# Performance work log

Measured on AMD Instinct MI355X. Metric: run time of the kernel, lower is better.

## Reference

```python
import jax, jax.numpy as jnp
import numpy as np
from jax import lax


def setup_inputs() -> dict:
    key = jax.random.key(0)
    ks = jax.random.split(key, 6)
    B, C, H, W, K = 4, 4, 64, 64, 8192
    return {
        "x": jax.random.normal(ks[0], (B, C, H, W), dtype=jnp.float32),
        "prequant_w": jax.random.normal(ks[1], (C, C), dtype=jnp.float32) * 0.5,
        "prequant_b": jax.random.normal(ks[2], (C,), dtype=jnp.float32) * 0.1,
        "codebook": jax.random.normal(ks[3], (K, C), dtype=jnp.float32),
        "postquant_w": jax.random.normal(ks[4], (C, C), dtype=jnp.float32) * 0.5,
        "postquant_b": jax.random.normal(ks[5], (C,), dtype=jnp.float32) * 0.1,
    }


def reference(x, prequant_w, prequant_b, codebook, postquant_w, postquant_b):
    # x: [B, C, H, W] = encoder_out output (pre-prequant latent)
    B, C, H, W = x.shape
    N = H * W

    # prequant 1x1 conv
    q_in = jnp.einsum("bchw,oc->bohw", x, prequant_w) + prequant_b[None, :, None, None]
    feat_q = q_in.reshape(B, C, N).transpose(0, 2, 1)  # [B, N, C] (quant_in)
    feat_e = x.reshape(B, C, N).transpose(0, 2, 1)     # [B, N, C] ('out' in torch code)

    # cdist (p=2); argmin is invariant under sqrt so use squared distances
    # [B, N, K]
    sq_dist = (
        jnp.sum(feat_q * feat_q, axis=-1, keepdims=True)
        - 2.0 * jnp.einsum("bnc,kc->bnk", feat_q, codebook)
        + jnp.sum(codebook * codebook, axis=-1)
    )
    closest_idx = jnp.argmin(sq_dist, axis=-1)  # [B, N]

    quant = codebook[closest_idx]  # gather -> [B, N, C]

    codebook_loss = jnp.mean((quant - lax.stop_gradient(feat_e)) ** 2)
    commitment_loss = jnp.mean((lax.stop_gradient(quant) - feat_e) ** 2)

    # straight-through estimator
    st = feat_e + lax.stop_gradient(quant - feat_e)
    quant_map = st.transpose(0, 2, 1).reshape(B, C, H, W)

    # postquant 1x1 conv (first op of decode())
    dec_in = jnp.einsum("bchw,oc->bohw", quant_map, postquant_w) + postquant_b[None, :, None, None]

    return dec_in, codebook_loss, commitment_loss, closest_idx.reshape(B, H, W)
```

## Files before the change

### kernel.cpp

```cpp
#include <hip/hip_runtime.h>

#define BB 4
#define CC 4
#define NN 4096
#define KK 8192
#define NPOS 16384
#define SLICES 4
#define SLICE_K (KK / SLICES)

#define OUT_LOSS 65536
#define OUT_IDX  65538

#define LOSS_BYTE_OFF (NPOS * SLICES * 8)

typedef float v2f __attribute__((ext_vector_type(2)));

__device__ __forceinline__ unsigned int fkey(float s) {
    unsigned int u = __float_as_uint(s);
    return (u & 0x80000000u) ? ~u : (u | 0x80000000u);
}

__global__ __launch_bounds__(256) void vq_search(const float* __restrict__ x,
                                                 const float* __restrict__ pw,
                                                 const float* __restrict__ pb,
                                                 const float* __restrict__ cb,
                                                 unsigned long long* __restrict__ keys_ws) {
    __shared__ unsigned long long keys[4][8][64];

    const int tid   = threadIdx.x;
    const int lane  = tid & 63;
    const int wave  = tid >> 6;
    const int slice = blockIdx.x & (SLICES - 1);
    const int pg    = blockIdx.x >> 2;
    const int pos0  = (pg * 4 + wave) * 8;
    const int k0    = slice * SLICE_K;

    float q[8][4], qq[8];
#pragma unroll
    for (int p = 0; p < 8; ++p) {
        int pos = pos0 + p;
        int b = pos >> 12, n = pos & 4095;
        const float* xb = x + b * (CC * NN) + n;
        float xv0 = xb[0], xv1 = xb[NN], xv2 = xb[2 * NN], xv3 = xb[3 * NN];
#pragma unroll
        for (int o = 0; o < 4; ++o) {
            float t = fmaf(pw[o * 4 + 0], xv0, 0.0f);
            t = fmaf(pw[o * 4 + 1], xv1, t);
            t = fmaf(pw[o * 4 + 2], xv2, t);
            t = fmaf(pw[o * 4 + 3], xv3, t);
            q[p][o] = __fadd_rn(t, pb[o]);
        }
        float s = __fmul_rn(q[p][0], q[p][0]);
        s = __fadd_rn(s, __fmul_rn(q[p][1], q[p][1]));
        s = __fadd_rn(s, __fmul_rn(q[p][2], q[p][2]));
        s = __fadd_rn(s, __fmul_rn(q[p][3], q[p][3]));
        qq[p] = s;
    }

    v2f q2[4][4], qq2[4];
#pragma unroll
    for (int g = 0; g < 4; ++g) {
#pragma unroll
        for (int c = 0; c < 4; ++c) q2[g][c] = (v2f){q[2 * g][c], q[2 * g + 1][c]};
        qq2[g] = (v2f){qq[2 * g], qq[2 * g + 1]};
    }

    float best[8];
    int   bi[8];
#pragma unroll
    for (int p = 0; p < 8; ++p) { best[p] = __int_as_float(0x7f800000); bi[p] = 0; }

    const float4* cb4 = (const float4*)cb;

#pragma unroll 2
    for (int k = k0 + lane; k < k0 + SLICE_K; k += 64) {
        float4 e = cb4[k];
        float nk = __fmul_rn(e.x, e.x);
        nk = __fadd_rn(nk, __fmul_rn(e.y, e.y));
        nk = __fadd_rn(nk, __fmul_rn(e.z, e.z));
        nk = __fadd_rn(nk, __fmul_rn(e.w, e.w));
        v2f nk2 = (v2f){nk, nk};
        v2f ex = (v2f){e.x, e.x}, ey = (v2f){e.y, e.y};
        v2f ez = (v2f){e.z, e.z}, ew = (v2f){e.w, e.w};
#pragma unroll
        for (int g = 0; g < 4; ++g) {
            v2f d = q2[g][0] * ex;
            d = __builtin_elementwise_fma(q2[g][1], ey, d);
            d = __builtin_elementwise_fma(q2[g][2], ez, d);
            d = __builtin_elementwise_fma(q2[g][3], ew, d);
            v2f s = __builtin_elementwise_fma((v2f){-2.0f, -2.0f}, d, qq2[g]);
            s = s + nk2;
            if (s.x < best[2 * g])     { best[2 * g]     = s.x; bi[2 * g]     = k; }
            if (s.y < best[2 * g + 1]) { best[2 * g + 1] = s.y; bi[2 * g + 1] = k; }
        }
    }

#pragma unroll
    for (int p = 0; p < 8; ++p)
        keys[wave][p][lane] =
            ((unsigned long long)fkey(best[p]) << 32) | (unsigned int)bi[p];
    __syncthreads();

    if (tid < 32) {
        int w = tid >> 3, p = tid & 7;
        unsigned long long bk = ~0ull;
#pragma unroll 4
        for (int i = 0; i < 64; ++i) {
            unsigned long long c = keys[w][p][i ^ tid];
            bk = (c < bk) ? c : bk;
        }
        int pos = (pg * 4 + w) * 8 + p;
        keys_ws[pos * SLICES + slice] = bk;
    }
}

__global__ __launch_bounds__(256) void vq_epi(const float* __restrict__ x,
                                              const float* __restrict__ cb,
                                              const float* __restrict__ qw,
                                              const float* __restrict__ qb,
                                              const unsigned long long* __restrict__ keys_ws,
                                              float* __restrict__ lossp,
                                              float* __restrict__ out) {
    __shared__ float red[256];
    const int tid = threadIdx.x;
    const int pos = blockIdx.x * 256 + tid;

    unsigned long long bk = keys_ws[pos * SLICES + 0];
    unsigned long long c1 = keys_ws[pos * SLICES + 1];
    unsigned long long c2 = keys_ws[pos * SLICES + 2];
    unsigned long long c3 = keys_ws[pos * SLICES + 3];
    bk = (c1 < bk) ? c1 : bk;
    bk = (c2 < bk) ? c2 : bk;
    bk = (c3 < bk) ? c3 : bk;
    int idx = (int)(bk & 0xFFFFFFFFull);

    int b = pos >> 12, n = pos & 4095;
    const float4* cb4 = (const float4*)cb;
    float4 e = cb4[idx];

    const float* xb = x + b * (CC * NN) + n;
    float xv0 = xb[0], xv1 = xb[NN], xv2 = xb[2 * NN], xv3 = xb[3 * NN];

    float s0 = __fadd_rn(xv0, __fsub_rn(e.x, xv0));
    float s1 = __fadd_rn(xv1, __fsub_rn(e.y, xv1));
    float s2 = __fadd_rn(xv2, __fsub_rn(e.z, xv2));
    float s3 = __fadd_rn(xv3, __fsub_rn(e.w, xv3));

#pragma unroll
    for (int o = 0; o < 4; ++o) {
        float t = fmaf(qw[o * 4 + 0], s0, 0.0f);
        t = fmaf(qw[o * 4 + 1], s1, t);
        t = fmaf(qw[o * 4 + 2], s2, t);
        t = fmaf(qw[o * 4 + 3], s3, t);
        t = __fadd_rn(t, qb[o]);
        out[b * (CC * NN) + o * NN + n] = t;
    }

    out[OUT_IDX + b * NN + n] = (float)idx;

    float d0 = __fsub_rn(e.x, xv0), d1 = __fsub_rn(e.y, xv1);
    float d2 = __fsub_rn(e.z, xv2), d3 = __fsub_rn(e.w, xv3);
    float lp = __fmul_rn(d0, d0);
    lp = __fadd_rn(lp, __fmul_rn(d1, d1));
    lp = __fadd_rn(lp, __fmul_rn(d2, d2));
    lp = __fadd_rn(lp, __fmul_rn(d3, d3));

    red[tid] = lp;
    __syncthreads();
#pragma unroll
    for (int s = 128; s > 0; s >>= 1) {
        if (tid < s) red[tid] += red[tid + s];
        __syncthreads();
    }
    if (tid == 0) lossp[blockIdx.x] = red[0];
}

__global__ void vq_fin(const float* __restrict__ lossp, float* __restrict__ out) {
    if (threadIdx.x == 0) {
        float s = 0.0f;
        for (int i = 0; i < 64; ++i) s += lossp[i];
        s *= (1.0f / (float)(NPOS * CC));
        out[OUT_LOSS + 0] = s;
        out[OUT_LOSS + 1] = s;
    }
}

extern "C" void kernel_launch(void* const* d_in, const int* in_sizes, int n_in,
                              void* d_out, int out_size, void* d_ws, size_t ws_size,
                              hipStream_t stream) {
    const float* x  = (const float*)d_in[0];
    const float* pw = (const float*)d_in[1];
    const float* pb = (const float*)d_in[2];
    const float* cb = (const float*)d_in[3];
    const float* qw = (const float*)d_in[4];
    const float* qb = (const float*)d_in[5];
    float* out = (float*)d_out;

    unsigned long long* keys_ws = (unsigned long long*)d_ws;
    float* lossp = (float*)((char*)d_ws + LOSS_BYTE_OFF);

    vq_search<<<(NPOS / 32) * SLICES, 256, 0, stream>>>(x, pw, pb, cb, keys_ws);
    vq_epi<<<NPOS / 256, 256, 0, stream>>>(x, cb, qw, qb, keys_ws, lossp, out);
    vq_fin<<<1, 64, 0, stream>>>(lossp, out);
}
```

Baseline: 103.3 us.

## Precompute codebook norms and prequant features in a separate pre-kernel

Adds a vq_pre kernel that computes the per-code squared norms and the prequant-projected features (with their squared norms) once and writes them to workspace. The search kernel, now launched as single-wave 64-thread blocks, loads these precomputed values instead of recomputing the codebook norm on every iteration in every block. It also tracks a loop counter instead of the full code index and does the final reduction with cross-lane shuffles. This removes redundant norm arithmetic from the hot loop at the cost of an extra kernel launch, an extra load per iteration, and much smaller blocks.

```diff
diff --git a/kernel.cpp b/kernel.cpp
--- a/kernel.cpp
+++ b/kernel.cpp
@@ -7,11 +7,15 @@
 #define NPOS 16384
 #define SLICES 4
 #define SLICE_K (KK / SLICES)
+#define ITERS (SLICE_K / 64)
 
 #define OUT_LOSS 65536
 #define OUT_IDX  65538
 
-#define LOSS_BYTE_OFF (NPOS * SLICES * 8)
+#define KEYS_BYTES (NPOS * SLICES * 8)
+#define QPRE_BYTE_OFF KEYS_BYTES
+#define NRM_BYTE_OFF  (QPRE_BYTE_OFF + 8192 * 16 * 4)
+#define LOSS_BYTE_OFF (NRM_BYTE_OFF + 8192 * 4)
 
 typedef float v2f __attribute__((ext_vector_type(2)));
 
@@ -20,66 +24,96 @@
     return (u & 0x80000000u) ? ~u : (u | 0x80000000u);
 }
 
-__global__ __launch_bounds__(256) void vq_search(const float* __restrict__ x,
-                                                 const float* __restrict__ pw,
-                                                 const float* __restrict__ pb,
-                                                 const float* __restrict__ cb,
-                                                 unsigned long long* __restrict__ keys_ws) {
-    __shared__ unsigned long long keys[4][8][64];
-
-    const int tid   = threadIdx.x;
-    const int lane  = tid & 63;
-    const int wave  = tid >> 6;
-    const int slice = blockIdx.x & (SLICES - 1);
-    const int pg    = blockIdx.x >> 2;
-    const int pos0  = (pg * 4 + wave) * 8;
+__device__ __forceinline__ unsigned long long shflx_u64(unsigned long long v, int m) {
+    unsigned int lo = __shfl_xor((unsigned int)v, m, 64);
+    unsigned int hi = __shfl_xor((unsigned int)(v >> 32), m, 64);
+    return ((unsigned long long)hi << 32) | lo;
+}
+
+__global__ __launch_bounds__(256) void vq_pre(const float* __restrict__ x,
+                                              const float* __restrict__ pw,
+                                              const float* __restrict__ pb,
+                                              const float* __restrict__ cb,
+                                              float* __restrict__ qpre,
+                                              float* __restrict__ nrm) {
+    int t = blockIdx.x * 256 + threadIdx.x;
+
+    const float* e = cb + t * 4;
+    float n0 = __fmul_rn(e[0], e[0]);
+    n0 = __fadd_rn(n0, __fmul_rn(e[1], e[1]));
+    n0 = __fadd_rn(n0, __fmul_rn(e[2], e[2]));
+    n0 = __fadd_rn(n0, __fmul_rn(e[3], e[3]));
+    nrm[t] = n0;
+
+    int pos = 2 * t;
+    int b = pos >> 12, n = pos & 4095;
+    const float2* px = (const float2*)(x + b * (CC * NN) + n);
+    float2 xv0 = px[0], xv1 = px[NN / 2], xv2 = px[NN], xv3 = px[3 * NN / 2];
+
+    float qs[2][4], qqs[2];
+#pragma unroll
+    for (int h = 0; h < 2; ++h) {
+        float a0 = h ? xv0.y : xv0.x, a1 = h ? xv1.y : xv1.x;
+        float a2 = h ? xv2.y : xv2.x, a3 = h ? xv3.y : xv3.x;
+#pragma unroll
+        for (int o = 0; o < 4; ++o) {
+            float tt = fmaf(pw[o * 4 + 0], a0, 0.0f);
+            tt = fmaf(pw[o * 4 + 1], a1, tt);
+            tt = fmaf(pw[o * 4 + 2], a2, tt);
+            tt = fmaf(pw[o * 4 + 3], a3, tt);
+            qs[h][o] = __fadd_rn(tt, pb[o]);
+        }
+        float s = __fmul_rn(qs[h][0], qs[h][0]);
+        s = __fadd_rn(s, __fmul_rn(qs[h][1], qs[h][1]));
+        s = __fadd_rn(s, __fmul_rn(qs[h][2], qs[h][2]));
+        s = __fadd_rn(s, __fmul_rn(qs[h][3], qs[h][3]));
+        qqs[h] = s;
+    }
+
+    float4* o4 = (float4*)(qpre + t * 16);
+    o4[0] = make_float4(qs[0][0], qs[1][0], qs[0][1], qs[1][1]);
+    o4[1] = make_float4(qs[0][2], qs[1][2], qs[0][3], qs[1][3]);
+    ((float2*)(qpre + t * 16 + 8))[0] = make_float2(qqs[0], qqs[1]);
+}
+
+__global__ __launch_bounds__(64) void vq_search(const float* __restrict__ cb,
+                                                const float* __restrict__ qpre,
+                                                const float* __restrict__ nrm,
+                                                unsigned long long* __restrict__ keys_ws) {
+    __shared__ unsigned long long keys[8][64];
+
+    const int lane  = threadIdx.x;
+    const int gid   = blockIdx.x;
+    const int slice = gid & (SLICES - 1);
+    const int pg    = gid >> 2;
     const int k0    = slice * SLICE_K;
 
-    float q[8][4], qq[8];
-#pragma unroll
-    for (int p = 0; p < 8; ++p) {
-        int pos = pos0 + p;
-        int b = pos >> 12, n = pos & 4095;
-        const float* xb = x + b * (CC * NN) + n;
-        float xv0 = xb[0], xv1 = xb[NN], xv2 = xb[2 * NN], xv3 = xb[3 * NN];
-#pragma unroll
-        for (int o = 0; o < 4; ++o) {
-            float t = fmaf(pw[o * 4 + 0], xv0, 0.0f);
-            t = fmaf(pw[o * 4 + 1], xv1, t);
-            t = fmaf(pw[o * 4 + 2], xv2, t);
-            t = fmaf(pw[o * 4 + 3], xv3, t);
-            q[p][o] = __fadd_rn(t, pb[o]);
-        }
-        float s = __fmul_rn(q[p][0], q[p][0]);
-        s = __fadd_rn(s, __fmul_rn(q[p][1], q[p][1]));
-        s = __fadd_rn(s, __fmul_rn(q[p][2], q[p][2]));
-        s = __fadd_rn(s, __fmul_rn(q[p][3], q[p][3]));
-        qq[p] = s;
-    }
-
     v2f q2[4][4], qq2[4];
+    const float* qp = qpre + (pg * 4) * 16;
 #pragma unroll
     for (int g = 0; g < 4; ++g) {
-#pragma unroll
-        for (int c = 0; c < 4; ++c) q2[g][c] = (v2f){q[2 * g][c], q[2 * g + 1][c]};
-        qq2[g] = (v2f){qq[2 * g], qq[2 * g + 1]};
+        float4 a = ((const float4*)(qp + g * 16))[0];
+        float4 b = ((const float4*)(qp + g * 16))[1];
+        float2 c = ((const float2*)(qp + g * 16 + 8))[0];
+        q2[g][0] = (v2f){a.x, a.y};
+        q2[g][1] = (v2f){a.z, a.w};
+        q2[g][2] = (v2f){b.x, b.y};
+        q2[g][3] = (v2f){b.z, b.w};
+        qq2[g]   = (v2f){c.x, c.y};
     }
 
     float best[8];
-    int   bi[8];
-#pragma unroll
-    for (int p = 0; p < 8; ++p) { best[p] = __int_as_float(0x7f800000); bi[p] = 0; }
-
-    const float4* cb4 = (const float4*)cb;
+    int   bit_[8];
+#pragma unroll
+    for (int p = 0; p < 8; ++p) { best[p] = __int_as_float(0x7f800000); bit_[p] = 0; }
+
+    const float4* cb4 = (const float4*)cb + k0 + lane;
+    const float*  nr  = nrm + k0 + lane;
 
 #pragma unroll 2
-    for (int k = k0 + lane; k < k0 + SLICE_K; k += 64) {
-        float4 e = cb4[k];
-        float nk = __fmul_rn(e.x, e.x);
-        nk = __fadd_rn(nk, __fmul_rn(e.y, e.y));
-        nk = __fadd_rn(nk, __fmul_rn(e.z, e.z));
-        nk = __fadd_rn(nk, __fmul_rn(e.w, e.w));
-        v2f nk2 = (v2f){nk, nk};
+    for (int it = 0; it < ITERS; ++it) {
+        float4 e  = cb4[it * 64];
+        float  nk = nr[it * 64];
         v2f ex = (v2f){e.x, e.x}, ey = (v2f){e.y, e.y};
         v2f ez = (v2f){e.z, e.z}, ew = (v2f){e.w, e.w};
 #pragma unroll
@@ -89,29 +123,35 @@
             d = __builtin_elementwise_fma(q2[g][2], ez, d);
             d = __builtin_elementwise_fma(q2[g][3], ew, d);
             v2f s = __builtin_elementwise_fma((v2f){-2.0f, -2.0f}, d, qq2[g]);
-            s = s + nk2;
-            if (s.x < best[2 * g])     { best[2 * g]     = s.x; bi[2 * g]     = k; }
-            if (s.y < best[2 * g + 1]) { best[2 * g + 1] = s.y; bi[2 * g + 1] = k; }
+            float sx = __fadd_rn(s.x, nk);
+            float sy = __fadd_rn(s.y, nk);
+            if (sx < best[2 * g])     { best[2 * g]     = sx; bit_[2 * g]     = it; }
+            if (sy < best[2 * g + 1]) { best[2 * g + 1] = sy; bit_[2 * g + 1] = it; }
         }
     }
 
 #pragma unroll
-    for (int p = 0; p < 8; ++p)
-        keys[wave][p][lane] =
-            ((unsigned long long)fkey(best[p]) << 32) | (unsigned int)bi[p];
+    for (int p = 0; p < 8; ++p) {
+        int kfull = k0 + lane + (bit_[p] << 6);
+        keys[p][lane] = ((unsigned long long)fkey(best[p]) << 32) | (unsigned int)kfull;
+    }
     __syncthreads();
 
-    if (tid < 32) {
-        int w = tid >> 3, p = tid & 7;
-        unsigned long long bk = ~0ull;
-#pragma unroll 4
-        for (int i = 0; i < 64; ++i) {
-            unsigned long long c = keys[w][p][i ^ tid];
-            bk = (c < bk) ? c : bk;
-        }
-        int pos = (pg * 4 + w) * 8 + p;
-        keys_ws[pos * SLICES + slice] = bk;
-    }
+    int p  = lane >> 3;
+    int j0 = (lane & 7) << 3;
+    unsigned long long bk = keys[p][j0];
+#pragma unroll
+    for (int j = 1; j < 8; ++j) {
+        unsigned long long c = keys[p][j0 + j];
+        bk = (c < bk) ? c : bk;
+    }
+#pragma unroll
+    for (int m = 1; m < 8; m <<= 1) {
+        unsigned long long c = shflx_u64(bk, m);
+        bk = (c < bk) ? c : bk;
+    }
+    if ((lane & 7) == 0)
+        keys_ws[(pg * 8 + p) * SLICES + slice] = bk;
 }
 
 __global__ __launch_bounds__(256) void vq_epi(const float* __restrict__ x,
@@ -197,9 +237,12 @@
     float* out = (float*)d_out;
 
     unsigned long long* keys_ws = (unsigned long long*)d_ws;
+    float* qpre  = (float*)((char*)d_ws + QPRE_BYTE_OFF);
+    float* nrm   = (float*)((char*)d_ws + NRM_BYTE_OFF);
     float* lossp = (float*)((char*)d_ws + LOSS_BYTE_OFF);
 
-    vq_search<<<(NPOS / 32) * SLICES, 256, 0, stream>>>(x, pw, pb, cb, keys_ws);
+    vq_pre<<<32, 256, 0, stream>>>(x, pw, pb, cb, qpre, nrm);
+    vq_search<<<(NPOS / 8) * SLICES, 64, 0, stream>>>(cb, qpre, nrm, keys_ws);
     vq_epi<<<NPOS / 256, 256, 0, stream>>>(x, cb, qw, qb, keys_ws, lossp, out);
     vq_fin<<<1, 64, 0, stream>>>(lossp, out);
 }
```

After: 100.2 us. -3.0%, faster.
